# Kernel tuning notes

Hardware: AMD Instinct MI355X
Metric: run time of the kernel (lower is better)

Reference implementation:

```python
import jax, jax.numpy as jnp
import numpy as np

B, I, H = 65536, 128, 256


def setup_inputs() -> dict:
    key = jax.random.key(0)
    ks = jax.random.split(key, 8)
    return {
        "x_t": jax.random.normal(ks[0], (B, I), dtype=jnp.float32),
        "delta_t": jax.random.uniform(ks[1], (B, 1), dtype=jnp.float32),
        "h_prev": jax.random.normal(ks[2], (B, H), dtype=jnp.float32),
        "c_prev": jax.random.normal(ks[3], (B, H), dtype=jnp.float32),
        # stacked gate weights, order: s, f, i, T, u, o
        "Wh": jax.random.normal(ks[4], (6, H, H), dtype=jnp.float32) * 0.05,
        "Wx": jax.random.normal(ks[5], (6, H, I), dtype=jnp.float32) * 0.05,
        # s_t-input weights, order: f, i, T, u, o
        "Ws": jax.random.normal(ks[6], (5, H, H), dtype=jnp.float32) * 0.05,
        "Wst": jax.random.normal(ks[7], (H, 1), dtype=jnp.float32) * 0.05,
        "b": jnp.zeros((6, H), dtype=jnp.float32),
    }


def reference(x_t, delta_t, h_prev, c_prev, Wh, Wx, Ws, Wst, b):
    # Batched GEMMs over the 6 gates (nn.Linear: y = x @ W.T)
    pre_h = jnp.einsum('bi,goi->gbo', h_prev, Wh)      # [6,B,H]
    pre_x = jnp.einsum('bi,goi->gbo', x_t, Wx)         # [6,B,H]
    s_t = jnp.tanh(pre_h[0] + pre_x[0] + delta_t @ Wst.T + b[0])
    pre_s = jnp.einsum('bi,goi->gbo', s_t, Ws)         # [5,B,H]
    g = pre_h[1:] + pre_x[1:] + pre_s + b[1:, None, :]  # [5,B,H] f,i,T,u,o
    f_t = jax.nn.sigmoid(g[0])
    i_t = jax.nn.sigmoid(g[1])
    T_t = jax.nn.sigmoid(g[2])
    zeta = jnp.tanh(g[3])
    o_t = jax.nn.sigmoid(g[4])
    c_t = f_t * c_prev + i_t * zeta + T_t * s_t
    h_tilde = o_t * jnp.tanh(c_t)
    return (h_tilde, c_t)
```

## Files before the change

kernel.cpp:

```cpp
#include <hip/hip_runtime.h>
#include <hip/hip_bf16.h>


constexpr int Btot = 65536;
constexpr int H    = 256;
constexpr int I    = 128;
constexpr int K1   = 384;
constexpr int BT   = 64;
constexpr int NTHR = 1024;
constexpr int REG1 = 40960;
constexpr int SOFF = 24576;

typedef __bf16 bf16x8  __attribute__((ext_vector_type(8)));
typedef float  f32x16  __attribute__((ext_vector_type(16)));
typedef unsigned short ushort8 __attribute__((ext_vector_type(8)));

__device__ __forceinline__ unsigned short f2bf(float f) {
    unsigned u = __builtin_bit_cast(unsigned, f);
    u += 0x7fffu + ((u >> 16) & 1u);
    return (unsigned short)(u >> 16);
}
__device__ __forceinline__ float bf2f(unsigned short s) {
    return __builtin_bit_cast(float, ((unsigned)s) << 16);
}
__device__ __forceinline__ float sigm(float x) {
    return __builtin_amdgcn_rcpf(1.0f + exp2f(-1.4426950408889634f * x));
}
__device__ __forceinline__ float tanh_f(float x) {
    return 1.0f - 2.0f * __builtin_amdgcn_rcpf(1.0f + exp2f(2.8853900817779268f * x));
}

__global__ void convert_w(const float* __restrict__ Wh, const float* __restrict__ Wx,
                          const float* __restrict__ Ws, unsigned short* __restrict__ w0,
                          unsigned short* __restrict__ wg) {
    const int t  = blockIdx.x * blockDim.x + threadIdx.x;
    const int N0 = 48 * 2048;
    const int N1 = 5 * 80 * 2048;
    if (t < N0) {
        const int k8 = t >> 11, rem = t & 2047;
        const int col = rem >> 3, e = rem & 7;
        const int k = k8 * 8 + e;
        const float v = (k < H) ? Wh[col * H + k] : Wx[col * I + (k - H)];
        w0[t] = f2bf(v);
    } else if (t < N0 + N1) {
        const int u   = t - N0;
        const int g1  = u / 163840;
        const int rem = u - g1 * 163840;
        const int k8  = rem >> 11;
        const int r2  = rem & 2047;
        const int col = r2 >> 3, e = r2 & 7;
        const int k   = k8 * 8 + e;
        const int g   = g1 + 1;
        float v;
        if (k < H)        v = Wh[g * H * H + col * H + k];
        else if (k < K1)  v = Wx[g * H * I + col * I + (k - H)];
        else              v = Ws[g1 * H * H + col * H + (k - K1)];
        wg[u] = f2bf(v);
    }
}

template<int NIT>
__device__ __forceinline__ void gemm1(const unsigned char* Ab, int abase,
        const unsigned short* __restrict__ Wp, f32x16& acc) {
    bf16x8 b[2], a[2];
    #pragma unroll
    for (int i = 0; i < 2; ++i) {
        b[i] = *(const bf16x8*)(Wp + i * 4096);
        a[i] = *(const bf16x8*)(Ab + abase + i * 1024);
    }
    #pragma unroll
    for (int i = 0; i < NIT; ++i) {
        const bf16x8 av = a[i & 1], bv = b[i & 1];
        if (i + 2 < NIT) {
            a[i & 1] = *(const bf16x8*)(Ab + abase + (i + 2) * 1024);
            b[i & 1] = *(const bf16x8*)(Wp + (i + 2) * 4096);
        }
        acc = __builtin_amdgcn_mfma_f32_32x32x16_bf16(av, bv, acc, 0, 0, 0);
    }
}

__global__ __launch_bounds__(NTHR, 4) void thlstm_fused(
        const float* __restrict__ x_t, const float* __restrict__ delta_t,
        const float* __restrict__ h_prev, const float* __restrict__ c_prev,
        const float* __restrict__ Wst, const float* __restrict__ bias,
        const unsigned short* __restrict__ w0, const unsigned short* __restrict__ wg,
        float* __restrict__ out) {
    __shared__ __align__(16) unsigned char Abuf[81920];
    const int tid = threadIdx.x;
    const int b0  = blockIdx.x * BT;

    #pragma unroll
    for (int it = 0; it < 3; ++it) {
        const int c   = it * NTHR + tid;
        const int k8  = c >> 6, row = c & 63;
        const float* src = (k8 < 32) ? (h_prev + (size_t)(b0 + row) * H + k8 * 8)
                                     : (x_t    + (size_t)(b0 + row) * I + (k8 - 32) * 8);
        const float4 v0 = ((const float4*)src)[0];
        const float4 v1 = ((const float4*)src)[1];
        ushort8 p;
        p[0] = f2bf(v0.x); p[1] = f2bf(v0.y); p[2] = f2bf(v0.z); p[3] = f2bf(v0.w);
        p[4] = f2bf(v1.x); p[5] = f2bf(v1.y); p[6] = f2bf(v1.z); p[7] = f2bf(v1.w);
        *(ushort8*)(Abuf + (row >> 5) * REG1 + (k8 * 32 + (row & 31)) * 16) = p;
    }
    __syncthreads();

    const int lane  = tid & 63;
    const int wv    = tid >> 6;
    const int rg    = wv >> 3;
    const int half  = lane >> 5;
    const int l31   = lane & 31;
    const int ocol  = (wv & 7) * 32 + l31;
    const int rowb  = rg * 32;
    const int rbase = 4 * half;
    const int abase = rg * REG1 + half * 512 + l31 * 16;
    const int wlo   = half * 2048 + ocol * 8;
    const int sbase = rg * REG1 + SOFF + ((ocol >> 3) * 32) * 16 + (ocol & 7) * 2;

    {
        f32x16 acc;
        #pragma unroll
        for (int r = 0; r < 16; ++r) acc[r] = 0.f;
        gemm1<24>(Abuf, abase, w0 + wlo, acc);
        const float wst = Wst[ocol];
        const float bs  = bias[ocol];
        #pragma unroll
        for (int r = 0; r < 16; ++r) {
            const int mrow = (r & 3) + 8 * (r >> 2) + rbase;
            const float sv = tanh_f(acc[r] + delta_t[b0 + rowb + mrow] * wst + bs);
            *(unsigned short*)(Abuf + sbase + mrow * 16) = f2bf(sv);
        }
    }
    __syncthreads();

    float    cacc[16];
    unsigned ipk[8];

    {
        f32x16 ac;
        #pragma unroll
        for (int r = 0; r < 16; ++r) ac[r] = 0.f;
        gemm1<40>(Abuf, abase, wg + 0 * 163840 + wlo, ac);
        const float bg = bias[1 * H + ocol];
        #pragma unroll
        for (int r = 0; r < 16; ++r) {
            const int mrow = (r & 3) + 8 * (r >> 2) + rbase;
            const size_t idx = (size_t)(b0 + rowb + mrow) * H + ocol;
            cacc[r] = sigm(ac[r] + bg) * c_prev[idx];
        }
    }
    {
        f32x16 ac;
        #pragma unroll
        for (int r = 0; r < 16; ++r) ac[r] = 0.f;
        gemm1<40>(Abuf, abase, wg + 2 * 163840 + wlo, ac);
        const float bg = bias[3 * H + ocol];
        #pragma unroll
        for (int r = 0; r < 16; ++r) {
            const int mrow = (r & 3) + 8 * (r >> 2) + rbase;
            const float sv = bf2f(*(const unsigned short*)(Abuf + sbase + mrow * 16));
            cacc[r] += sigm(ac[r] + bg) * sv;
        }
    }
    {
        f32x16 ac;
        #pragma unroll
        for (int r = 0; r < 16; ++r) ac[r] = 0.f;
        gemm1<40>(Abuf, abase, wg + 1 * 163840 + wlo, ac);
        const float bg = bias[2 * H + ocol];
        float tmpf = 0.f;
        #pragma unroll
        for (int r = 0; r < 16; ++r) {
            const float sg = sigm(ac[r] + bg);
            if ((r & 1) == 0) tmpf = sg;
            else ipk[r >> 1] = (unsigned)f2bf(tmpf) | ((unsigned)f2bf(sg) << 16);
        }
    }
    {
        f32x16 ac;
        #pragma unroll
        for (int r = 0; r < 16; ++r) ac[r] = 0.f;
        gemm1<40>(Abuf, abase, wg + 3 * 163840 + wlo, ac);
        const float bg = bias[4 * H + ocol];
        #pragma unroll
        for (int r = 0; r < 16; ++r) {
            const float iv = bf2f((unsigned short)((ipk[r >> 1] >> ((r & 1) * 16)) & 0xffffu));
            cacc[r] += iv * tanh_f(ac[r] + bg);
        }
    }
    {
        f32x16 ac;
        #pragma unroll
        for (int r = 0; r < 16; ++r) ac[r] = 0.f;
        gemm1<40>(Abuf, abase, wg + 4 * 163840 + wlo, ac);
        const float bg = bias[5 * H + ocol];
        #pragma unroll
        for (int r = 0; r < 16; ++r) {
            const int mrow = (r & 3) + 8 * (r >> 2) + rbase;
            const size_t idx = (size_t)(b0 + rowb + mrow) * H + ocol;
            const float c = cacc[r];
            out[idx] = sigm(ac[r] + bg) * tanh_f(c);
            out[(size_t)Btot * H + idx] = c;
        }
    }
}

extern "C" void kernel_launch(void* const* d_in, const int* in_sizes, int n_in,
                              void* d_out, int out_size, void* d_ws, size_t ws_size,
                              hipStream_t stream) {
    (void)in_sizes; (void)n_in; (void)out_size; (void)ws_size;
    const float* x_t    = (const float*)d_in[0];
    const float* delta  = (const float*)d_in[1];
    const float* h_prev = (const float*)d_in[2];
    const float* c_prev = (const float*)d_in[3];
    const float* Wh     = (const float*)d_in[4];
    const float* Wx     = (const float*)d_in[5];
    const float* Ws     = (const float*)d_in[6];
    const float* Wst    = (const float*)d_in[7];
    const float* bias   = (const float*)d_in[8];
    float* out = (float*)d_out;

    unsigned short* w0 = (unsigned short*)d_ws;
    unsigned short* wg = w0 + 48 * 2048;

    const int total = 48 * 2048 + 5 * 80 * 2048;
    convert_w<<<(total + 255) / 256, 256, 0, stream>>>(Wh, Wx, Ws, w0, wg);
    thlstm_fused<<<Btot / BT, NTHR, 0, stream>>>(x_t, delta, h_prev, c_prev,
                                                 Wst, bias, w0, wg, out);
}
```

Measured before the change: 221.4 us.

## Pair gate GEMMs to share A-fragment loads and keep partial cell state in LDS

```diff
diff --git a/kernel.cpp b/kernel.cpp
--- a/kernel.cpp
+++ b/kernel.cpp
@@ -10,6 +10,7 @@
 constexpr int NTHR = 1024;
 constexpr int REG1 = 40960;
 constexpr int SOFF = 24576;
+constexpr int COFF = 81920;
 
 typedef __bf16 bf16x8  __attribute__((ext_vector_type(8)));
 typedef float  f32x16  __attribute__((ext_vector_type(16)));
@@ -79,13 +80,37 @@
     }
 }
 
+template<int NIT>
+__device__ __forceinline__ void gemm2g(const unsigned char* Ab, int abase,
+        const unsigned short* __restrict__ Wp0, const unsigned short* __restrict__ Wp1,
+        f32x16& acc0, f32x16& acc1) {
+    bf16x8 b0[2], b1[2], a[2];
+    #pragma unroll
+    for (int i = 0; i < 2; ++i) {
+        b0[i] = *(const bf16x8*)(Wp0 + i * 4096);
+        b1[i] = *(const bf16x8*)(Wp1 + i * 4096);
+        a[i]  = *(const bf16x8*)(Ab + abase + i * 1024);
+    }
+    #pragma unroll
+    for (int i = 0; i < NIT; ++i) {
+        const bf16x8 av = a[i & 1], bv0 = b0[i & 1], bv1 = b1[i & 1];
+        if (i + 2 < NIT) {
+            a[i & 1]  = *(const bf16x8*)(Ab + abase + (i + 2) * 1024);
+            b0[i & 1] = *(const bf16x8*)(Wp0 + (i + 2) * 4096);
+            b1[i & 1] = *(const bf16x8*)(Wp1 + (i + 2) * 4096);
+        }
+        acc0 = __builtin_amdgcn_mfma_f32_32x32x16_bf16(av, bv0, acc0, 0, 0, 0);
+        acc1 = __builtin_amdgcn_mfma_f32_32x32x16_bf16(av, bv1, acc1, 0, 0, 0);
+    }
+}
+
 __global__ __launch_bounds__(NTHR, 4) void thlstm_fused(
         const float* __restrict__ x_t, const float* __restrict__ delta_t,
         const float* __restrict__ h_prev, const float* __restrict__ c_prev,
         const float* __restrict__ Wst, const float* __restrict__ bias,
         const unsigned short* __restrict__ w0, const unsigned short* __restrict__ wg,
         float* __restrict__ out) {
-    __shared__ __align__(16) unsigned char Abuf[81920];
+    __shared__ __align__(16) unsigned char Abuf[114688];
     const int tid = threadIdx.x;
     const int b0  = blockIdx.x * BT;
 
@@ -115,6 +140,7 @@
     const int abase = rg * REG1 + half * 512 + l31 * 16;
     const int wlo   = half * 2048 + ocol * 8;
     const int sbase = rg * REG1 + SOFF + ((ocol >> 3) * 32) * 16 + (ocol & 7) * 2;
+    const int cbase = COFF + (ocol >> 3) * 1024 + (ocol & 7) * 2;
 
     {
         f32x16 acc;
@@ -132,59 +158,37 @@
     }
     __syncthreads();
 
-    float    cacc[16];
-    unsigned ipk[8];
-
-    {
-        f32x16 ac;
-        #pragma unroll
-        for (int r = 0; r < 16; ++r) ac[r] = 0.f;
-        gemm1<40>(Abuf, abase, wg + 0 * 163840 + wlo, ac);
-        const float bg = bias[1 * H + ocol];
-        #pragma unroll
-        for (int r = 0; r < 16; ++r) {
-            const int mrow = (r & 3) + 8 * (r >> 2) + rbase;
-            const size_t idx = (size_t)(b0 + rowb + mrow) * H + ocol;
-            cacc[r] = sigm(ac[r] + bg) * c_prev[idx];
-        }
-    }
-    {
-        f32x16 ac;
-        #pragma unroll
-        for (int r = 0; r < 16; ++r) ac[r] = 0.f;
-        gemm1<40>(Abuf, abase, wg + 2 * 163840 + wlo, ac);
-        const float bg = bias[3 * H + ocol];
-        #pragma unroll
-        for (int r = 0; r < 16; ++r) {
-            const int mrow = (r & 3) + 8 * (r >> 2) + rbase;
+    {
+        f32x16 acf, acT;
+        #pragma unroll
+        for (int r = 0; r < 16; ++r) { acf[r] = 0.f; acT[r] = 0.f; }
+        gemm2g<40>(Abuf, abase, wg + 0 * 163840 + wlo, wg + 2 * 163840 + wlo, acf, acT);
+        const float bgf = bias[1 * H + ocol];
+        const float bgT = bias[3 * H + ocol];
+        #pragma unroll
+        for (int r = 0; r < 16; ++r) {
+            const int mrow = (r & 3) + 8 * (r >> 2) + rbase;
+            const int grow = rowb + mrow;
+            const size_t idx = (size_t)(b0 + grow) * H + ocol;
             const float sv = bf2f(*(const unsigned short*)(Abuf + sbase + mrow * 16));
-            cacc[r] += sigm(ac[r] + bg) * sv;
-        }
-    }
-    {
-        f32x16 ac;
-        #pragma unroll
-        for (int r = 0; r < 16; ++r) ac[r] = 0.f;
-        gemm1<40>(Abuf, abase, wg + 1 * 163840 + wlo, ac);
-        const float bg = bias[2 * H + ocol];
-        float tmpf = 0.f;
-        #pragma unroll
-        for (int r = 0; r < 16; ++r) {
-            const float sg = sigm(ac[r] + bg);
-            if ((r & 1) == 0) tmpf = sg;
-            else ipk[r >> 1] = (unsigned)f2bf(tmpf) | ((unsigned)f2bf(sg) << 16);
-        }
-    }
-    {
-        f32x16 ac;
-        #pragma unroll
-        for (int r = 0; r < 16; ++r) ac[r] = 0.f;
-        gemm1<40>(Abuf, abase, wg + 3 * 163840 + wlo, ac);
-        const float bg = bias[4 * H + ocol];
-        #pragma unroll
-        for (int r = 0; r < 16; ++r) {
-            const float iv = bf2f((unsigned short)((ipk[r >> 1] >> ((r & 1) * 16)) & 0xffffu));
-            cacc[r] += iv * tanh_f(ac[r] + bg);
+            const float cv = sigm(acf[r] + bgf) * c_prev[idx] + sigm(acT[r] + bgT) * sv;
+            *(unsigned short*)(Abuf + cbase + grow * 16) = f2bf(cv);
+        }
+    }
+    {
+        f32x16 aci, acu;
+        #pragma unroll
+        for (int r = 0; r < 16; ++r) { aci[r] = 0.f; acu[r] = 0.f; }
+        gemm2g<40>(Abuf, abase, wg + 1 * 163840 + wlo, wg + 3 * 163840 + wlo, aci, acu);
+        const float bgi = bias[2 * H + ocol];
+        const float bgu = bias[4 * H + ocol];
+        #pragma unroll
+        for (int r = 0; r < 16; ++r) {
+            const int mrow = (r & 3) + 8 * (r >> 2) + rbase;
+            const int grow = rowb + mrow;
+            const float co = bf2f(*(const unsigned short*)(Abuf + cbase + grow * 16));
+            const float cv = co + sigm(aci[r] + bgi) * tanh_f(acu[r] + bgu);
+            *(unsigned short*)(Abuf + cbase + grow * 16) = f2bf(cv);
         }
     }
     {
@@ -196,8 +200,9 @@
         #pragma unroll
         for (int r = 0; r < 16; ++r) {
             const int mrow = (r & 3) + 8 * (r >> 2) + rbase;
-            const size_t idx = (size_t)(b0 + rowb + mrow) * H + ocol;
-            const float c = cacc[r];
+            const int grow = rowb + mrow;
+            const size_t idx = (size_t)(b0 + grow) * H + ocol;
+            const float c = bf2f(*(const unsigned short*)(Abuf + cbase + grow * 16));
             out[idx] = sigm(ac[r] + bg) * tanh_f(c);
             out[(size_t)Btot * H + idx] = c;
         }
```

Result: no change. 219.5 us (-0.9%).
